# Optimization experiments

Measured on AMD Instinct MI355X. Metric: run time of the kernel, lower is better.

The kernel has to match this reference:

```python
import jax, jax.numpy as jnp
import numpy as np

B, I, C, U, S = 256, 128, 1024, 32, 16  # batch, in_units, in_channels, num_units, unit_size
NUM_ITERS = 3

def setup_inputs() -> dict:
    key = jax.random.key(0)
    k1, k2 = jax.random.split(key)
    x = jax.random.normal(k1, (B, I, C), dtype=jnp.float32)
    W = jax.random.normal(k2, (1, C, U, S, I), dtype=jnp.float32)
    return {"x": x, "W": W}

def _squash(s):
    # s: (b, u, s); original squashes over dim=2 of (b,1,U,S,1), i.e. the num_units axis
    mag_sq = jnp.sum(s * s, axis=1, keepdims=True)
    mag = jnp.sqrt(mag_sq)
    return mag_sq / (1.0 + mag_sq) * (s / mag)

def reference(x, W):
    # x: (b, in_units, in_channels) -> (b, c, i)
    xT = jnp.swapaxes(x, 1, 2)
    # u_hat[b,c,u,s] = sum_i W[0,c,u,s,i] * xT[b,c,i]  (replaces torch.cat broadcast + matmul)
    u_hat = jnp.einsum('cusi,bci->bcus', W[0], xT)
    b_ij = jnp.zeros((1, C, U, 1), dtype=x.dtype)
    v_j = None
    for _ in range(NUM_ITERS):
        # softmax over axis 0 of size 1 -> all ones (faithful to original quirk)
        c_ij = jax.nn.softmax(b_ij, axis=0)
        s_j = jnp.einsum('cu,bcus->bus', c_ij[0, :, :, 0], u_hat)
        v_j = _squash(s_j)
        # agreement: mean over batch of <u_hat, v_j> along unit_size
        u_vj = jnp.einsum('bcus,bus->cu', u_hat, v_j) / B
        b_ij = b_ij + u_vj[None, :, :, None]
    return v_j[..., None]  # (b, num_units, unit_size, 1) == v_j.squeeze(1)
```

## Files before the change

kernel.cpp:

```cpp
#include <hip/hip_runtime.h>
#include <hip/hip_bf16.h>
#include <stdint.h>

#define B_DIM 256
#define I_DIM 128
#define C_DIM 1024
#define N_DIM 512
#define KC    (C_DIM * I_DIM)

typedef __bf16 bf16;
typedef __attribute__((ext_vector_type(4))) __bf16 bf16x4;
typedef __attribute__((ext_vector_type(8))) __bf16 bf16x8;
typedef __attribute__((ext_vector_type(4))) float f32x4;

__device__ __forceinline__ void async_copy16(const bf16* g, short* l) {
  __builtin_amdgcn_global_load_lds(
      (const __attribute__((address_space(1))) uint32_t*)g,
      (__attribute__((address_space(3))) uint32_t*)l, 16, 0, 0);
}

__global__ void __launch_bounds__(256)
transpose_cast(const float* __restrict__ x, bf16* __restrict__ xT) {
  __shared__ float tile[64][65];
  const int c0 = blockIdx.x * 64;
  const int i0 = blockIdx.y * 64;
  const int b  = blockIdx.z;
  const int t  = threadIdx.x;
  const int sub = t >> 4;
  const int cg  = t & 15;
  const float* xb = x + (size_t)b * (I_DIM * C_DIM);
#pragma unroll
  for (int r = 0; r < 4; ++r) {
    const int i = r * 16 + sub;
    const float4 v = *(const float4*)&xb[(size_t)(i0 + i) * C_DIM + c0 + cg * 4];
    tile[i][cg * 4 + 0] = v.x; tile[i][cg * 4 + 1] = v.y;
    tile[i][cg * 4 + 2] = v.z; tile[i][cg * 4 + 3] = v.w;
  }
  __syncthreads();
  bf16* xTb = xT + (size_t)b * KC;
#pragma unroll
  for (int r = 0; r < 4; ++r) {
    const int c = r * 16 + sub;
    bf16x4 o;
    o[0] = (bf16)tile[cg * 4 + 0][c];
    o[1] = (bf16)tile[cg * 4 + 1][c];
    o[2] = (bf16)tile[cg * 4 + 2][c];
    o[3] = (bf16)tile[cg * 4 + 3][c];
    *(bf16x4*)&xTb[(size_t)(c0 + c) * I_DIM + i0 + cg * 4] = o;
  }
}

__global__ void __launch_bounds__(512, 4)
gemm_kernel(const bf16* __restrict__ xT, const float* __restrict__ W,
            float* __restrict__ sj) {
  __shared__ short Alds[B_DIM * I_DIM];
  const int tid  = threadIdx.x;
  const int lane = tid & 63;
  const int wave = tid >> 6;
  const int wm   = wave >> 1;
  const int wn   = wave & 1;
  const int l15  = lane & 15;
  const int lq   = lane >> 4;
  const int n0   = blockIdx.x * 64;
  const int c0   = blockIdx.y * 16;
  const int row_st   = tid >> 4;
  const int chunk_st = tid & 15;

  f32x4 acc[4][2] = {};

  for (int cc = 0; cc < 16; ++cc) {
    const int c = c0 + cc;
    const float* Wc = W + (size_t)c * (N_DIM * I_DIM);
    __syncthreads();

    float4 wraw[2][2][2];
#pragma unroll
    for (int nt = 0; nt < 2; ++nt) {
      const float* wp = Wc + (size_t)(n0 + wn * 32 + nt * 16 + l15) * I_DIM + lq * 8;
      wraw[0][nt][0] = *(const float4*)wp;
      wraw[0][nt][1] = *(const float4*)(wp + 4);
    }

#pragma unroll
    for (int r = 0; r < 8; ++r) {
      const int m    = r * 32 + row_st;
      const int csrc = chunk_st ^ (m & 15);
      const bf16* g  = xT + (size_t)m * KC + (size_t)c * I_DIM + csrc * 8;
      async_copy16(g, &Alds[m * I_DIM + chunk_st * 8]);
    }
    __syncthreads();

#pragma unroll
    for (int ks = 0; ks < 4; ++ks) {
      const int cur = ks & 1;
      if (ks < 3) {
        const int i0n = (ks + 1) * 32;
#pragma unroll
        for (int nt = 0; nt < 2; ++nt) {
          const float* wp = Wc + (size_t)(n0 + wn * 32 + nt * 16 + l15) * I_DIM + i0n + lq * 8;
          wraw[cur ^ 1][nt][0] = *(const float4*)wp;
          wraw[cur ^ 1][nt][1] = *(const float4*)(wp + 4);
        }
      }
      const int i0 = ks * 32;
      bf16x8 a[4];
#pragma unroll
      for (int mt = 0; mt < 4; ++mt) {
        const int m  = wm * 64 + mt * 16 + l15;
        const int st = ((i0 >> 3) + lq) ^ l15;
        a[mt] = *(const bf16x8*)&Alds[m * I_DIM + st * 8];
      }
      bf16x8 b[2];
#pragma unroll
      for (int nt = 0; nt < 2; ++nt) {
        const float4 w0 = wraw[cur][nt][0];
        const float4 w1 = wraw[cur][nt][1];
        bf16x8 bb;
        bb[0] = (bf16)w0.x; bb[1] = (bf16)w0.y;
        bb[2] = (bf16)w0.z; bb[3] = (bf16)w0.w;
        bb[4] = (bf16)w1.x; bb[5] = (bf16)w1.y;
        bb[6] = (bf16)w1.z; bb[7] = (bf16)w1.w;
        b[nt] = bb;
      }
#pragma unroll
      for (int mt = 0; mt < 4; ++mt)
#pragma unroll
        for (int nt = 0; nt < 2; ++nt)
          acc[mt][nt] = __builtin_amdgcn_mfma_f32_16x16x32_bf16(
              a[mt], b[nt], acc[mt][nt], 0, 0, 0);
    }
  }

#pragma unroll
  for (int mt = 0; mt < 4; ++mt) {
#pragma unroll
    for (int nt = 0; nt < 2; ++nt) {
      const int n = n0 + wn * 32 + nt * 16 + l15;
#pragma unroll
      for (int r = 0; r < 4; ++r) {
        const int brow = wm * 64 + mt * 16 + lq * 4 + r;
        atomicAdd(&sj[(size_t)brow * N_DIM + n], acc[mt][nt][r]);
      }
    }
  }
}

__global__ void __launch_bounds__(512)
squash_kernel(const float* __restrict__ sj, float* __restrict__ out) {
  __shared__ float sm[512];
  const int b = blockIdx.x;
  const int t = threadIdx.x;
  const float v = sj[(size_t)b * N_DIM + t];
  sm[t] = v * v;
  __syncthreads();
#pragma unroll
  for (int off = 256; off >= 16; off >>= 1) {
    if (t < off) sm[t] += sm[t + off];
    __syncthreads();
  }
  const float msq   = sm[t & 15];
  const float scale = sqrtf(msq) / (1.0f + msq);
  out[(size_t)b * N_DIM + t] = v * scale;
}

extern "C" void kernel_launch(void* const* d_in, const int* in_sizes, int n_in,
                              void* d_out, int out_size, void* d_ws, size_t ws_size,
                              hipStream_t stream) {
  const float* x = (const float*)d_in[0];
  const float* W = (const float*)d_in[1];
  float* out = (float*)d_out;

  bf16*  xT = (bf16*)d_ws;
  float* sj = (float*)((char*)d_ws + (size_t)B_DIM * KC * sizeof(bf16));

  hipMemsetAsync(sj, 0, (size_t)B_DIM * N_DIM * sizeof(float), stream);
  transpose_cast<<<dim3(C_DIM / 64, I_DIM / 64, B_DIM), 256, 0, stream>>>(x, xT);
  gemm_kernel<<<dim3(8, 64), 512, 0, stream>>>(xT, W, sj);
  squash_kernel<<<B_DIM, 512, 0, stream>>>(sj, out);
}
```

Baseline: 550.1 us.

## Triple-buffer A and W tiles via async LDS loads in split-K GEMM

Restructures the GEMM main loop into a three-stage software pipeline. Both the bf16 activation tile and the fp32 W tile now go through async global-to-LDS copies with XOR swizzles, in 64-wide K steps. The grid shrinks to 256 blocks, each covering 32 channels, with a remapped block index, which halves the number of atomic partial-sum adds. The transpose kernel now writes 8-wide bf16 vectors. The deeper pipeline aims to hide global load latency, at the cost of more LDS per block and lower occupancy (launch bounds 512,2).

```diff
diff --git a/kernel.cpp b/kernel.cpp
--- a/kernel.cpp
+++ b/kernel.cpp
@@ -7,13 +7,14 @@
 #define C_DIM 1024
 #define N_DIM 512
 #define KC    (C_DIM * I_DIM)
+#define WC    (N_DIM * I_DIM)
 
 typedef __bf16 bf16;
 typedef __attribute__((ext_vector_type(4))) __bf16 bf16x4;
 typedef __attribute__((ext_vector_type(8))) __bf16 bf16x8;
 typedef __attribute__((ext_vector_type(4))) float f32x4;
 
-__device__ __forceinline__ void async_copy16(const bf16* g, short* l) {
+__device__ __forceinline__ void async_copy16(const void* g, void* l) {
   __builtin_amdgcn_global_load_lds(
       (const __attribute__((address_space(1))) uint32_t*)g,
       (__attribute__((address_space(3))) uint32_t*)l, 16, 0, 0);
@@ -39,21 +40,80 @@
   __syncthreads();
   bf16* xTb = xT + (size_t)b * KC;
 #pragma unroll
-  for (int r = 0; r < 4; ++r) {
-    const int c = r * 16 + sub;
-    bf16x4 o;
-    o[0] = (bf16)tile[cg * 4 + 0][c];
-    o[1] = (bf16)tile[cg * 4 + 1][c];
-    o[2] = (bf16)tile[cg * 4 + 2][c];
-    o[3] = (bf16)tile[cg * 4 + 3][c];
-    *(bf16x4*)&xTb[(size_t)(c0 + c) * I_DIM + i0 + cg * 4] = o;
-  }
-}
-
-__global__ void __launch_bounds__(512, 4)
+  for (int r = 0; r < 2; ++r) {
+    const int c  = r * 32 + (t >> 3);
+    const int ic = (t & 7) * 8;
+    bf16x8 o;
+#pragma unroll
+    for (int k = 0; k < 8; ++k) o[k] = (bf16)tile[ic + k][c];
+    *(bf16x8*)&xTb[(size_t)(c0 + c) * I_DIM + i0 + ic] = o;
+  }
+}
+
+__device__ __forceinline__ void stage_step(
+    const bf16* __restrict__ xT, const float* __restrict__ W,
+    short* Asl, float* Wsl, int tid, int c, int h, int n0) {
+  const int ch = tid & 7;
+  const size_t abase = (size_t)c * I_DIM + h * 64;
+#pragma unroll
+  for (int p = 0; p < 4; ++p) {
+    const int m   = p * 64 + (tid >> 3);
+    const int csw = ch ^ (m & 7);
+    async_copy16(xT + (size_t)m * KC + abase + csw * 8,
+                 &Asl[(p * 512 + tid) * 8]);
+  }
+  const int s = tid & 15;
+  const size_t wbase = (size_t)c * WC + h * 64;
+#pragma unroll
+  for (int p = 0; p < 2; ++p) {
+    const int n   = p * 32 + (tid >> 4);
+    const int ssw = s ^ (n & 7);
+    async_copy16(W + wbase + (size_t)(n0 + n) * I_DIM + ssw * 4,
+                 &Wsl[(p * 512 + tid) * 4]);
+  }
+}
+
+__device__ __forceinline__ void compute_step(
+    const short* Asl, const float* Wsl,
+    int wm, int wn, int l15, int lq, f32x4 (&acc)[4][2]) {
+#pragma unroll
+  for (int ks = 0; ks < 2; ++ks) {
+    bf16x8 a[4];
+#pragma unroll
+    for (int mt = 0; mt < 4; ++mt) {
+      const int m  = wm * 64 + mt * 16 + l15;
+      const int ch = (ks * 4 + lq) ^ (l15 & 7);
+      a[mt] = *(const bf16x8*)&Asl[m * 64 + ch * 8];
+    }
+    bf16x8 b[2];
+#pragma unroll
+    for (int nt = 0; nt < 2; ++nt) {
+      const int n  = wn * 32 + nt * 16 + l15;
+      const int s0 = (ks * 8 + lq * 2)     ^ (l15 & 7);
+      const int s1 = (ks * 8 + lq * 2 + 1) ^ (l15 & 7);
+      const f32x4 lo = *(const f32x4*)&Wsl[n * 64 + s0 * 4];
+      const f32x4 hi = *(const f32x4*)&Wsl[n * 64 + s1 * 4];
+      bf16x8 bb;
+      bb[0] = (bf16)lo[0]; bb[1] = (bf16)lo[1];
+      bb[2] = (bf16)lo[2]; bb[3] = (bf16)lo[3];
+      bb[4] = (bf16)hi[0]; bb[5] = (bf16)hi[1];
+      bb[6] = (bf16)hi[2]; bb[7] = (bf16)hi[3];
+      b[nt] = bb;
+    }
+#pragma unroll
+    for (int mt = 0; mt < 4; ++mt)
+#pragma unroll
+      for (int nt = 0; nt < 2; ++nt)
+        acc[mt][nt] = __builtin_amdgcn_mfma_f32_16x16x32_bf16(
+            a[mt], b[nt], acc[mt][nt], 0, 0, 0);
+  }
+}
+
+__global__ void __launch_bounds__(512, 2)
 gemm_kernel(const bf16* __restrict__ xT, const float* __restrict__ W,
             float* __restrict__ sj) {
-  __shared__ short Alds[B_DIM * I_DIM];
+  __shared__ short As[3][B_DIM * 64];
+  __shared__ float Ws[3][64 * 64];
   const int tid  = threadIdx.x;
   const int lane = tid & 63;
   const int wave = tid >> 6;
@@ -61,75 +121,40 @@
   const int wn   = wave & 1;
   const int l15  = lane & 15;
   const int lq   = lane >> 4;
-  const int n0   = blockIdx.x * 64;
-  const int c0   = blockIdx.y * 16;
-  const int row_st   = tid >> 4;
-  const int chunk_st = tid & 15;
+
+  const int g   = blockIdx.x;
+  const int n0  = ((g >> 3) & 7) * 64;
+  const int cch = (g & 7) * 4 + (g >> 6);
+  const int c0  = cch * 32;
 
   f32x4 acc[4][2] = {};
 
-  for (int cc = 0; cc < 16; ++cc) {
-    const int c = c0 + cc;
-    const float* Wc = W + (size_t)c * (N_DIM * I_DIM);
-    __syncthreads();
-
-    float4 wraw[2][2][2];
-#pragma unroll
-    for (int nt = 0; nt < 2; ++nt) {
-      const float* wp = Wc + (size_t)(n0 + wn * 32 + nt * 16 + l15) * I_DIM + lq * 8;
-      wraw[0][nt][0] = *(const float4*)wp;
-      wraw[0][nt][1] = *(const float4*)(wp + 4);
-    }
-
-#pragma unroll
-    for (int r = 0; r < 8; ++r) {
-      const int m    = r * 32 + row_st;
-      const int csrc = chunk_st ^ (m & 15);
-      const bf16* g  = xT + (size_t)m * KC + (size_t)c * I_DIM + csrc * 8;
-      async_copy16(g, &Alds[m * I_DIM + chunk_st * 8]);
-    }
-    __syncthreads();
-
-#pragma unroll
-    for (int ks = 0; ks < 4; ++ks) {
-      const int cur = ks & 1;
-      if (ks < 3) {
-        const int i0n = (ks + 1) * 32;
-#pragma unroll
-        for (int nt = 0; nt < 2; ++nt) {
-          const float* wp = Wc + (size_t)(n0 + wn * 32 + nt * 16 + l15) * I_DIM + i0n + lq * 8;
-          wraw[cur ^ 1][nt][0] = *(const float4*)wp;
-          wraw[cur ^ 1][nt][1] = *(const float4*)(wp + 4);
-        }
-      }
-      const int i0 = ks * 32;
-      bf16x8 a[4];
-#pragma unroll
-      for (int mt = 0; mt < 4; ++mt) {
-        const int m  = wm * 64 + mt * 16 + l15;
-        const int st = ((i0 >> 3) + lq) ^ l15;
-        a[mt] = *(const bf16x8*)&Alds[m * I_DIM + st * 8];
-      }
-      bf16x8 b[2];
-#pragma unroll
-      for (int nt = 0; nt < 2; ++nt) {
-        const float4 w0 = wraw[cur][nt][0];
-        const float4 w1 = wraw[cur][nt][1];
-        bf16x8 bb;
-        bb[0] = (bf16)w0.x; bb[1] = (bf16)w0.y;
-        bb[2] = (bf16)w0.z; bb[3] = (bf16)w0.w;
-        bb[4] = (bf16)w1.x; bb[5] = (bf16)w1.y;
-        bb[6] = (bf16)w1.z; bb[7] = (bf16)w1.w;
-        b[nt] = bb;
-      }
-#pragma unroll
-      for (int mt = 0; mt < 4; ++mt)
-#pragma unroll
-        for (int nt = 0; nt < 2; ++nt)
-          acc[mt][nt] = __builtin_amdgcn_mfma_f32_16x16x32_bf16(
-              a[mt], b[nt], acc[mt][nt], 0, 0, 0);
-    }
-  }
+  short *Aa = As[0], *Ab = As[1], *Ac = As[2];
+  float *Wa = Ws[0], *Wb = Ws[1], *Wc = Ws[2];
+
+  stage_step(xT, W, Aa, Wa, tid, c0, 0, n0);
+  stage_step(xT, W, Ab, Wb, tid, c0, 1, n0);
+
+#pragma unroll 1
+  for (int t = 0; t < 62; ++t) {
+    const int tn = t + 2;
+    stage_step(xT, W, Ac, Wc, tid, c0 + (tn >> 1), tn & 1, n0);
+    asm volatile("s_waitcnt vmcnt(12)" ::: "memory");
+    __builtin_amdgcn_sched_barrier(0);
+    __builtin_amdgcn_s_barrier();
+    compute_step(Aa, Wa, wm, wn, l15, lq, acc);
+    __builtin_amdgcn_s_barrier();
+    short* ta = Aa; Aa = Ab; Ab = Ac; Ac = ta;
+    float* tw = Wa; Wa = Wb; Wb = Wc; Wc = tw;
+  }
+  asm volatile("s_waitcnt vmcnt(6)" ::: "memory");
+  __builtin_amdgcn_sched_barrier(0);
+  __builtin_amdgcn_s_barrier();
+  compute_step(Aa, Wa, wm, wn, l15, lq, acc);
+  asm volatile("s_waitcnt vmcnt(0)" ::: "memory");
+  __builtin_amdgcn_sched_barrier(0);
+  __builtin_amdgcn_s_barrier();
+  compute_step(Ab, Wb, wm, wn, l15, lq, acc);
 
 #pragma unroll
   for (int mt = 0; mt < 4; ++mt) {
@@ -175,6 +200,6 @@
 
   hipMemsetAsync(sj, 0, (size_t)B_DIM * N_DIM * sizeof(float), stream);
   transpose_cast<<<dim3(C_DIM / 64, I_DIM / 64, B_DIM), 256, 0, stream>>>(x, xT);
-  gemm_kernel<<<dim3(8, 64), 512, 0, stream>>>(xT, W, sj);
+  gemm_kernel<<<dim3(256), 512, 0, stream>>>(xT, W, sj);
   squash_kernel<<<B_DIM, 512, 0, stream>>>(sj, out);
 }
```

After: 492.7 us. -10.4%, faster.
